# Performance work log

Measured on AMD Instinct MI355X. Metric: run time of the kernel, lower is better.

## Reference

```python
import jax, jax.numpy as jnp
import numpy as np

N, F, V, E = 16384, 39, 100000, 16
H1, H2 = 400, 400
EPS = 1e-5

def setup_inputs() -> dict:
    key = jax.random.key(0)
    ks = jax.random.split(key, 12)
    xi = jax.random.randint(ks[0], (N, F, 1), 0, V)  # indices per field
    xv = jax.random.uniform(ks[1], (N, F), dtype=jnp.float32)
    # stacked per-field embedding tables (each table has V+1 rows)
    emb1 = jax.random.normal(ks[2], (F, V + 1), dtype=jnp.float32)          # 1st-order
    emb2 = jax.random.normal(ks[3], (F, V + 1, E), dtype=jnp.float32)       # 2nd-order
    D = F * E
    W1 = jax.random.normal(ks[4], (D, H1), dtype=jnp.float32) / np.sqrt(D)
    b1 = jnp.zeros((H1,), jnp.float32)
    g1 = jnp.ones((H1,), jnp.float32)
    be1 = jnp.zeros((H1,), jnp.float32)
    W2 = jax.random.normal(ks[5], (H1, H2), dtype=jnp.float32) / np.sqrt(H1)
    b2 = jnp.zeros((H2,), jnp.float32)
    g2 = jnp.ones((H2,), jnp.float32)
    be2 = jnp.zeros((H2,), jnp.float32)
    bias = jax.random.normal(ks[6], (1,), dtype=jnp.float32)
    return dict(xi=xi, xv=xv, emb1=emb1, emb2=emb2, W1=W1, b1=b1, g1=g1, be1=be1,
                W2=W2, b2=b2, g2=g2, be2=be2, bias=bias)

def _batchnorm(x, g, b):
    # BatchNorm1d in training mode: batch mean/var (biased)
    mu = x.mean(0)
    var = x.var(0)
    return g * (x - mu) * jax.lax.rsqrt(var + EPS) + b

def reference(xi, xv, emb1, emb2, W1, b1, g1, be1, W2, b2, g2, be2, bias):
    idx = xi[:, :, 0]                     # (N, F)
    f_ids = jnp.arange(F)[None, :]        # (1, F)
    e1 = emb1[f_ids, idx] * xv            # (N, F): per-field 1st-order term
    e2 = emb2[f_ids, idx] * xv[:, :, None]  # (N, F, E)
    s = e2.sum(axis=1)                    # (N, E) sum of embeddings
    fm2 = 0.5 * (s * s - (e2 * e2).sum(axis=1))  # (N, E) FM 2nd-order
    deep = e2.reshape(e2.shape[0], F * E)
    h = _batchnorm(deep @ W1 + b1, g1, be1)       # dropout = identity (eval)
    h = _batchnorm(h @ W2 + b2, g2, be2)
    return e1.sum(axis=1) + fm2.sum(axis=1) + h.sum(axis=1) + bias[0]
```

## Files before the change

### kernel.cpp

```cpp
#include <hip/hip_runtime.h>
#include <hip/hip_bf16.h>

#define Nn 16384
#define Ff 39
#define Vv 100000
#define Ee 16
#define Dd 624
#define Hh 400
#define EPSf 1e-5f

typedef short short8 __attribute__((ext_vector_type(8)));
typedef float floatx4 __attribute__((ext_vector_type(4)));

__device__ __forceinline__ float bf2f(unsigned short v) {
  union { unsigned int u; float f; } x; x.u = ((unsigned int)v) << 16; return x.f;
}

__global__ __launch_bounds__(256) void embed_kernel(
    const int* __restrict__ xi, const float* __restrict__ xv,
    const float* __restrict__ emb1, const float* __restrict__ emb2,
    const float* __restrict__ bias,
    __hip_bfloat16* __restrict__ deep, float* __restrict__ p) {
  __shared__ int   sidx[4][40];
  __shared__ float sxv[4][40];
  const int w = threadIdx.x >> 6;
  const int lane = threadIdx.x & 63;
  const int n = blockIdx.x * 4 + w;
  if (lane < Ff) {
    sidx[w][lane] = xi[n * Ff + lane];
    sxv[w][lane]  = xv[n * Ff + lane];
  }
  __syncthreads();

  float s_e = 0.f, sq_e = 0.f;
  #pragma unroll
  for (int j = lane; j < Dd; j += 64) {
    const int f = j >> 4;
    const long off = ((long)f * (Vv + 1) + sidx[w][f]) * Ee + (j & 15);
    const float v = emb2[off] * sxv[w][f];
    deep[(long)n * Dd + j] = __float2bfloat16(v);
    s_e += v; sq_e += v * v;
  }
  s_e  += __shfl_xor(s_e, 16);  sq_e += __shfl_xor(sq_e, 16);
  s_e  += __shfl_xor(s_e, 32);  sq_e += __shfl_xor(sq_e, 32);

  float val = (lane < Ee) ? 0.5f * (s_e * s_e - sq_e) : 0.f;
  if (lane < Ff)
    val += emb1[(long)lane * (Vv + 1) + sidx[w][lane]] * sxv[w][lane];
  #pragma unroll
  for (int d = 1; d < 64; d <<= 1) val += __shfl_xor(val, d);
  if (lane == 0) p[n] = val + bias[0];
}

__global__ __launch_bounds__(256) void gemm_bf16(
    const __hip_bfloat16* __restrict__ A, const __hip_bfloat16* __restrict__ Wt,
    const float* __restrict__ bias, __hip_bfloat16* __restrict__ C,
    float* __restrict__ s, float* __restrict__ ss, int K) {
  __shared__ uint4 As4[128 * 5];
  __shared__ uint4 Bs4[80 * 5];
  const int tid = threadIdx.x;
  const int n0 = blockIdx.x * 80;
  const int m0 = blockIdx.y * 128;
  const int w = tid >> 6, lane = tid & 63;
  const int lm = lane & 15, qd = lane >> 4;

  floatx4 acc[2][5];
  #pragma unroll
  for (int i = 0; i < 2; ++i)
    #pragma unroll
    for (int j = 0; j < 5; ++j)
      acc[i][j] = (floatx4){0.f, 0.f, 0.f, 0.f};

  const short* As_s = (const short*)As4;
  const short* Bs_s = (const short*)Bs4;
  const int nk = (K + 31) >> 5;

  for (int ks = 0; ks < nk; ++ks) {
    const int k0 = ks << 5;
    #pragma unroll
    for (int cc = 0; cc < 2; ++cc) {
      const int c = tid + cc * 256;
      const int m = c >> 2, kc = c & 3;
      const int k = k0 + kc * 8;
      uint4 v = make_uint4(0, 0, 0, 0);
      if (k < K) v = *(const uint4*)&A[(size_t)(m0 + m) * K + k];
      As4[m * 5 + kc] = v;
    }
    for (int c = tid; c < 320; c += 256) {
      const int n = c >> 2, kc = c & 3;
      const int k = k0 + kc * 8;
      uint4 v = make_uint4(0, 0, 0, 0);
      if (k < K) v = *(const uint4*)&Wt[(size_t)(n0 + n) * K + k];
      Bs4[n * 5 + kc] = v;
    }
    __syncthreads();
    const short8 a0 = *(const short8*)&As_s[(w * 32 + 0  + lm) * 40 + qd * 8];
    const short8 a1 = *(const short8*)&As_s[(w * 32 + 16 + lm) * 40 + qd * 8];
    #pragma unroll
    for (int nt = 0; nt < 5; ++nt) {
      const short8 b = *(const short8*)&Bs_s[(nt * 16 + lm) * 40 + qd * 8];
      acc[0][nt] = __builtin_amdgcn_mfma_f32_16x16x32_bf16(a0, b, acc[0][nt], 0, 0, 0);
      acc[1][nt] = __builtin_amdgcn_mfma_f32_16x16x32_bf16(a1, b, acc[1][nt], 0, 0, 0);
    }
    __syncthreads();
  }

  const int rb = m0 + w * 32 + qd * 4;
  #pragma unroll
  for (int nt = 0; nt < 5; ++nt) {
    const int col = n0 + nt * 16 + lm;
    const float bc = bias[col];
    float cs = 0.f, cq = 0.f;
    #pragma unroll
    for (int mt = 0; mt < 2; ++mt) {
      #pragma unroll
      for (int r = 0; r < 4; ++r) {
        const float v = acc[mt][nt][r] + bc;
        const __hip_bfloat16 hv = __float2bfloat16(v);
        C[(size_t)(rb + mt * 16 + r) * Hh + col] = hv;
        const float vf = __bfloat162float(hv);
        cs += vf; cq += vf * vf;
      }
    }
    cs += __shfl_xor(cs, 16); cq += __shfl_xor(cq, 16);
    cs += __shfl_xor(cs, 32); cq += __shfl_xor(cq, 32);
    if (lane < 16) { atomicAdd(&s[col], cs); atomicAdd(&ss[col], cq); }
  }
}

__global__ __launch_bounds__(256) void conv1_kernel(
    const float* __restrict__ W1, __hip_bfloat16* __restrict__ W1t) {
  const int n = blockIdx.x, t = threadIdx.x;
  for (int k = t; k < Dd; k += 256)
    W1t[(size_t)n * Dd + k] = __float2bfloat16(W1[(size_t)k * Hh + n]);
}

__global__ void a1c1_kernel(
    const float* __restrict__ s1, const float* __restrict__ ss1,
    const float* __restrict__ g1, const float* __restrict__ be1,
    float* __restrict__ a1, float* __restrict__ c1) {
  const int t = threadIdx.x;
  if (t < Hh) {
    const float mu = s1[t] * (1.f / Nn);
    const float var = ss1[t] * (1.f / Nn) - mu * mu;
    const float a = g1[t] * rsqrtf(var + EPSf);
    a1[t] = a;
    c1[t] = be1[t] - a * mu;
  }
}

__global__ __launch_bounds__(256) void prep2_kernel(
    const float* __restrict__ W2, const float* __restrict__ a1, const float* __restrict__ c1,
    const float* __restrict__ b2, __hip_bfloat16* __restrict__ W2t, float* __restrict__ b2p) {
  __shared__ float red[256];
  const int n = blockIdx.x, t = threadIdx.x;
  float acc = 0.f;
  for (int k = t; k < Hh; k += 256) {
    const float wv = W2[(size_t)k * Hh + n];
    W2t[(size_t)n * Hh + k] = __float2bfloat16(a1[k] * wv);
    acc += c1[k] * wv;
  }
  red[t] = acc; __syncthreads();
  for (int d = 128; d > 0; d >>= 1) { if (t < d) red[t] += red[t + d]; __syncthreads(); }
  if (t == 0) b2p[n] = b2[n] + red[0];
}

__global__ __launch_bounds__(512) void alpha_kernel(
    const float* __restrict__ s2, const float* __restrict__ ss2,
    const float* __restrict__ g2, const float* __restrict__ be2,
    float* __restrict__ alpha, float* __restrict__ c2) {
  __shared__ float red[512];
  const int t = threadIdx.x;
  float part = 0.f;
  if (t < Hh) {
    const float mu = s2[t] * (1.f / Nn);
    const float var = ss2[t] * (1.f / Nn) - mu * mu;
    const float al = g2[t] * rsqrtf(var + EPSf);
    alpha[t] = al;
    part = be2[t] - al * mu;
  }
  red[t] = part;
  __syncthreads();
  for (int d = 256; d > 0; d >>= 1) { if (t < d) red[t] += red[t + d]; __syncthreads(); }
  if (t == 0) c2[0] = red[0];
}

__global__ __launch_bounds__(256) void final_kernel(
    const __hip_bfloat16* __restrict__ x2, const float* __restrict__ alpha,
    const float* __restrict__ p, const float* __restrict__ c2,
    float* __restrict__ out) {
  const int w = threadIdx.x >> 6, lane = threadIdx.x & 63;
  const int n = blockIdx.x * 4 + w;
  const unsigned short* row = (const unsigned short*)(x2 + (size_t)n * Hh);
  float acc = 0.f;
  for (int h0 = lane * 4; h0 < Hh; h0 += 256) {
    const ushort4 u = *(const ushort4*)&row[h0];
    const float4 al = *(const float4*)&alpha[h0];
    acc += bf2f(u.x) * al.x + bf2f(u.y) * al.y + bf2f(u.z) * al.z + bf2f(u.w) * al.w;
  }
  #pragma unroll
  for (int d = 1; d < 64; d <<= 1) acc += __shfl_xor(acc, d);
  if (lane == 0) out[n] = p[n] + acc + c2[0];
}

extern "C" void kernel_launch(void* const* d_in, const int* in_sizes, int n_in,
                              void* d_out, int out_size, void* d_ws, size_t ws_size,
                              hipStream_t stream) {
  const int*   xi   = (const int*)d_in[0];
  const float* xv   = (const float*)d_in[1];
  const float* emb1 = (const float*)d_in[2];
  const float* emb2 = (const float*)d_in[3];
  const float* W1   = (const float*)d_in[4];
  const float* b1   = (const float*)d_in[5];
  const float* g1   = (const float*)d_in[6];
  const float* be1  = (const float*)d_in[7];
  const float* W2   = (const float*)d_in[8];
  const float* b2   = (const float*)d_in[9];
  const float* g2   = (const float*)d_in[10];
  const float* be2  = (const float*)d_in[11];
  const float* bias = (const float*)d_in[12];
  float* out = (float*)d_out;

  char* ws = (char*)d_ws;
  __hip_bfloat16* deep = (__hip_bfloat16*)ws;                  ws += (size_t)Nn * Dd * 2;
  __hip_bfloat16* x1b  = (__hip_bfloat16*)ws;                  ws += (size_t)Nn * Hh * 2;
  __hip_bfloat16* x2b  = (__hip_bfloat16*)ws;                  ws += (size_t)Nn * Hh * 2;
  __hip_bfloat16* W1t  = (__hip_bfloat16*)ws;                  ws += (size_t)Hh * Dd * 2;
  __hip_bfloat16* W2t  = (__hip_bfloat16*)ws;                  ws += (size_t)Hh * Hh * 2;
  float* p    = (float*)ws;  ws += (size_t)Nn * 4;
  float* s1   = (float*)ws;  ws += Hh * 4;
  float* ss1  = (float*)ws;  ws += Hh * 4;
  float* s2   = (float*)ws;  ws += Hh * 4;
  float* ss2  = (float*)ws;  ws += Hh * 4;
  float* a1   = (float*)ws;  ws += Hh * 4;
  float* c1   = (float*)ws;  ws += Hh * 4;
  float* alpha= (float*)ws;  ws += Hh * 4;
  float* b2p  = (float*)ws;  ws += Hh * 4;
  float* c2   = (float*)ws;  ws += 16;

  hipMemsetAsync(s1, 0, 4 * Hh * sizeof(float), stream);

  embed_kernel<<<Nn / 4, 256, 0, stream>>>(xi, xv, emb1, emb2, bias, deep, p);
  conv1_kernel<<<Hh, 256, 0, stream>>>(W1, W1t);

  gemm_bf16<<<dim3(5, Nn / 128), 256, 0, stream>>>(deep, W1t, b1, x1b, s1, ss1, Dd);
  a1c1_kernel<<<1, 512, 0, stream>>>(s1, ss1, g1, be1, a1, c1);
  prep2_kernel<<<Hh, 256, 0, stream>>>(W2, a1, c1, b2, W2t, b2p);

  gemm_bf16<<<dim3(5, Nn / 128), 256, 0, stream>>>(x1b, W2t, b2p, x2b, s2, ss2, Hh);
  alpha_kernel<<<1, 512, 0, stream>>>(s2, ss2, g2, be2, alpha, c2);

  final_kernel<<<Nn / 4, 256, 0, stream>>>(x2b, alpha, p, c2, out);
}
```

Baseline: 440.3 us.

## Fuse small prep kernels into neighbors and double GEMM K-tile to 64

Folds the W1 transpose and the stats zeroing into extra blocks of the embedding kernel, and drops the memset. The BN1 scale/shift computation moves into prep2 and the BN2 alpha/c2 computation into the final kernel, which removes several tiny launches and their serialization gaps. The GEMM now stages a K-step of 64 with padded LDS rows, halving barrier count per tile. In exchange, every final-kernel block recomputes the alpha reduction redundantly. For K=400 the last 64-wide step is partly zero-padded.

Result: no change. 432.5 us (-1.8%).

```diff
diff --git a/kernel.cpp b/kernel.cpp
--- a/kernel.cpp
+++ b/kernel.cpp
@@ -19,13 +19,25 @@
 __global__ __launch_bounds__(256) void embed_kernel(
     const int* __restrict__ xi, const float* __restrict__ xv,
     const float* __restrict__ emb1, const float* __restrict__ emb2,
-    const float* __restrict__ bias,
-    __hip_bfloat16* __restrict__ deep, float* __restrict__ p) {
+    const float* __restrict__ bias, const float* __restrict__ W1,
+    __hip_bfloat16* __restrict__ deep, float* __restrict__ p,
+    __hip_bfloat16* __restrict__ W1t, float* __restrict__ stats) {
+  const int b = blockIdx.x;
+  if (b >= 4096) {
+    if (b == 4496) {
+      for (int i = threadIdx.x; i < 1600; i += 256) stats[i] = 0.f;
+    } else {
+      const int n = b - 4096;
+      for (int k = threadIdx.x; k < Dd; k += 256)
+        W1t[(size_t)n * Dd + k] = __float2bfloat16(W1[(size_t)k * Hh + n]);
+    }
+    return;
+  }
   __shared__ int   sidx[4][40];
   __shared__ float sxv[4][40];
   const int w = threadIdx.x >> 6;
   const int lane = threadIdx.x & 63;
-  const int n = blockIdx.x * 4 + w;
+  const int n = b * 4 + w;
   if (lane < Ff) {
     sidx[w][lane] = xi[n * Ff + lane];
     sxv[w][lane]  = xv[n * Ff + lane];
@@ -56,8 +68,8 @@
     const __hip_bfloat16* __restrict__ A, const __hip_bfloat16* __restrict__ Wt,
     const float* __restrict__ bias, __hip_bfloat16* __restrict__ C,
     float* __restrict__ s, float* __restrict__ ss, int K) {
-  __shared__ uint4 As4[128 * 5];
-  __shared__ uint4 Bs4[80 * 5];
+  __shared__ uint4 As4[128 * 9];
+  __shared__ uint4 Bs4[80 * 9];
   const int tid = threadIdx.x;
   const int n0 = blockIdx.x * 80;
   const int m0 = blockIdx.y * 128;
@@ -73,34 +85,38 @@
 
   const short* As_s = (const short*)As4;
   const short* Bs_s = (const short*)Bs4;
-  const int nk = (K + 31) >> 5;
+  const int nk = (K + 63) >> 6;
 
   for (int ks = 0; ks < nk; ++ks) {
-    const int k0 = ks << 5;
-    #pragma unroll
-    for (int cc = 0; cc < 2; ++cc) {
+    const int k0 = ks << 6;
+    #pragma unroll
+    for (int cc = 0; cc < 4; ++cc) {
       const int c = tid + cc * 256;
-      const int m = c >> 2, kc = c & 3;
+      const int m = c >> 3, kc = c & 7;
       const int k = k0 + kc * 8;
       uint4 v = make_uint4(0, 0, 0, 0);
       if (k < K) v = *(const uint4*)&A[(size_t)(m0 + m) * K + k];
-      As4[m * 5 + kc] = v;
-    }
-    for (int c = tid; c < 320; c += 256) {
-      const int n = c >> 2, kc = c & 3;
+      As4[m * 9 + kc] = v;
+    }
+    for (int c = tid; c < 640; c += 256) {
+      const int n = c >> 3, kc = c & 7;
       const int k = k0 + kc * 8;
       uint4 v = make_uint4(0, 0, 0, 0);
       if (k < K) v = *(const uint4*)&Wt[(size_t)(n0 + n) * K + k];
-      Bs4[n * 5 + kc] = v;
+      Bs4[n * 9 + kc] = v;
     }
     __syncthreads();
-    const short8 a0 = *(const short8*)&As_s[(w * 32 + 0  + lm) * 40 + qd * 8];
-    const short8 a1 = *(const short8*)&As_s[(w * 32 + 16 + lm) * 40 + qd * 8];
-    #pragma unroll
-    for (int nt = 0; nt < 5; ++nt) {
-      const short8 b = *(const short8*)&Bs_s[(nt * 16 + lm) * 40 + qd * 8];
-      acc[0][nt] = __builtin_amdgcn_mfma_f32_16x16x32_bf16(a0, b, acc[0][nt], 0, 0, 0);
-      acc[1][nt] = __builtin_amdgcn_mfma_f32_16x16x32_bf16(a1, b, acc[1][nt], 0, 0, 0);
+    #pragma unroll
+    for (int h = 0; h < 2; ++h) {
+      const int ko = h * 32 + qd * 8;
+      const short8 a0 = *(const short8*)&As_s[(w * 32 + 0  + lm) * 72 + ko];
+      const short8 a1 = *(const short8*)&As_s[(w * 32 + 16 + lm) * 72 + ko];
+      #pragma unroll
+      for (int nt = 0; nt < 5; ++nt) {
+        const short8 b = *(const short8*)&Bs_s[(nt * 16 + lm) * 72 + ko];
+        acc[0][nt] = __builtin_amdgcn_mfma_f32_16x16x32_bf16(a0, b, acc[0][nt], 0, 0, 0);
+        acc[1][nt] = __builtin_amdgcn_mfma_f32_16x16x32_bf16(a1, b, acc[1][nt], 0, 0, 0);
+      }
     }
     __syncthreads();
   }
@@ -128,79 +144,66 @@
   }
 }
 
-__global__ __launch_bounds__(256) void conv1_kernel(
-    const float* __restrict__ W1, __hip_bfloat16* __restrict__ W1t) {
-  const int n = blockIdx.x, t = threadIdx.x;
-  for (int k = t; k < Dd; k += 256)
-    W1t[(size_t)n * Dd + k] = __float2bfloat16(W1[(size_t)k * Hh + n]);
-}
-
-__global__ void a1c1_kernel(
+__global__ __launch_bounds__(256) void prep2_kernel(
+    const float* __restrict__ W2,
     const float* __restrict__ s1, const float* __restrict__ ss1,
     const float* __restrict__ g1, const float* __restrict__ be1,
-    float* __restrict__ a1, float* __restrict__ c1) {
-  const int t = threadIdx.x;
-  if (t < Hh) {
-    const float mu = s1[t] * (1.f / Nn);
-    const float var = ss1[t] * (1.f / Nn) - mu * mu;
-    const float a = g1[t] * rsqrtf(var + EPSf);
-    a1[t] = a;
-    c1[t] = be1[t] - a * mu;
-  }
-}
-
-__global__ __launch_bounds__(256) void prep2_kernel(
-    const float* __restrict__ W2, const float* __restrict__ a1, const float* __restrict__ c1,
     const float* __restrict__ b2, __hip_bfloat16* __restrict__ W2t, float* __restrict__ b2p) {
+  __shared__ float sa1[Hh], sc1[Hh];
   __shared__ float red[256];
   const int n = blockIdx.x, t = threadIdx.x;
+  for (int k = t; k < Hh; k += 256) {
+    const float mu = s1[k] * (1.f / Nn);
+    const float var = ss1[k] * (1.f / Nn) - mu * mu;
+    const float a = g1[k] * rsqrtf(var + EPSf);
+    sa1[k] = a;
+    sc1[k] = be1[k] - a * mu;
+  }
+  __syncthreads();
   float acc = 0.f;
   for (int k = t; k < Hh; k += 256) {
     const float wv = W2[(size_t)k * Hh + n];
-    W2t[(size_t)n * Hh + k] = __float2bfloat16(a1[k] * wv);
-    acc += c1[k] * wv;
+    W2t[(size_t)n * Hh + k] = __float2bfloat16(sa1[k] * wv);
+    acc += sc1[k] * wv;
   }
   red[t] = acc; __syncthreads();
   for (int d = 128; d > 0; d >>= 1) { if (t < d) red[t] += red[t + d]; __syncthreads(); }
   if (t == 0) b2p[n] = b2[n] + red[0];
 }
 
-__global__ __launch_bounds__(512) void alpha_kernel(
+__global__ __launch_bounds__(256) void final_kernel(
+    const __hip_bfloat16* __restrict__ x2,
     const float* __restrict__ s2, const float* __restrict__ ss2,
     const float* __restrict__ g2, const float* __restrict__ be2,
-    float* __restrict__ alpha, float* __restrict__ c2) {
-  __shared__ float red[512];
+    const float* __restrict__ p, float* __restrict__ out) {
+  __shared__ float sal[Hh];
+  __shared__ float red[256];
   const int t = threadIdx.x;
   float part = 0.f;
-  if (t < Hh) {
-    const float mu = s2[t] * (1.f / Nn);
-    const float var = ss2[t] * (1.f / Nn) - mu * mu;
-    const float al = g2[t] * rsqrtf(var + EPSf);
-    alpha[t] = al;
-    part = be2[t] - al * mu;
-  }
-  red[t] = part;
+  for (int h = t; h < Hh; h += 256) {
+    const float mu = s2[h] * (1.f / Nn);
+    const float var = ss2[h] * (1.f / Nn) - mu * mu;
+    const float al = g2[h] * rsqrtf(var + EPSf);
+    sal[h] = al;
+    part += be2[h] - al * mu;
+  }
+  red[t] = part; __syncthreads();
+  for (int d = 128; d > 0; d >>= 1) { if (t < d) red[t] += red[t + d]; __syncthreads(); }
   __syncthreads();
-  for (int d = 256; d > 0; d >>= 1) { if (t < d) red[t] += red[t + d]; __syncthreads(); }
-  if (t == 0) c2[0] = red[0];
-}
-
-__global__ __launch_bounds__(256) void final_kernel(
-    const __hip_bfloat16* __restrict__ x2, const float* __restrict__ alpha,
-    const float* __restrict__ p, const float* __restrict__ c2,
-    float* __restrict__ out) {
-  const int w = threadIdx.x >> 6, lane = threadIdx.x & 63;
+  const float c2 = red[0];
+
+  const int w = t >> 6, lane = t & 63;
   const int n = blockIdx.x * 4 + w;
   const unsigned short* row = (const unsigned short*)(x2 + (size_t)n * Hh);
   float acc = 0.f;
   for (int h0 = lane * 4; h0 < Hh; h0 += 256) {
     const ushort4 u = *(const ushort4*)&row[h0];
-    const float4 al = *(const float4*)&alpha[h0];
-    acc += bf2f(u.x) * al.x + bf2f(u.y) * al.y + bf2f(u.z) * al.z + bf2f(u.w) * al.w;
+    acc += bf2f(u.x) * sal[h0] + bf2f(u.y) * sal[h0 + 1]
+         + bf2f(u.z) * sal[h0 + 2] + bf2f(u.w) * sal[h0 + 3];
   }
   #pragma unroll
   for (int d = 1; d < 64; d <<= 1) acc += __shfl_xor(acc, d);
-  if (lane == 0) out[n] = p[n] + acc + c2[0];
+  if (lane == 0) out[n] = p[n] + acc + c2;
 }
 
 extern "C" void kernel_launch(void* const* d_in, const int* in_sizes, int n_in,
@@ -222,33 +225,21 @@
   float* out = (float*)d_out;
 
   char* ws = (char*)d_ws;
-  __hip_bfloat16* deep = (__hip_bfloat16*)ws;                  ws += (size_t)Nn * Dd * 2;
-  __hip_bfloat16* x1b  = (__hip_bfloat16*)ws;                  ws += (size_t)Nn * Hh * 2;
-  __hip_bfloat16* x2b  = (__hip_bfloat16*)ws;                  ws += (size_t)Nn * Hh * 2;
-  __hip_bfloat16* W1t  = (__hip_bfloat16*)ws;                  ws += (size_t)Hh * Dd * 2;
-  __hip_bfloat16* W2t  = (__hip_bfloat16*)ws;                  ws += (size_t)Hh * Hh * 2;
+  __hip_bfloat16* deep = (__hip_bfloat16*)ws;  ws += (size_t)Nn * Dd * 2;
+  __hip_bfloat16* x1b  = (__hip_bfloat16*)ws;  ws += (size_t)Nn * Hh * 2;
+  __hip_bfloat16* x2b  = (__hip_bfloat16*)ws;  ws += (size_t)Nn * Hh * 2;
+  __hip_bfloat16* W1t  = (__hip_bfloat16*)ws;  ws += (size_t)Hh * Dd * 2;
+  __hip_bfloat16* W2t  = (__hip_bfloat16*)ws;  ws += (size_t)Hh * Hh * 2;
   float* p    = (float*)ws;  ws += (size_t)Nn * 4;
   float* s1   = (float*)ws;  ws += Hh * 4;
   float* ss1  = (float*)ws;  ws += Hh * 4;
   float* s2   = (float*)ws;  ws += Hh * 4;
   float* ss2  = (float*)ws;  ws += Hh * 4;
-  float* a1   = (float*)ws;  ws += Hh * 4;
-  float* c1   = (float*)ws;  ws += Hh * 4;
-  float* alpha= (float*)ws;  ws += Hh * 4;
   float* b2p  = (float*)ws;  ws += Hh * 4;
-  float* c2   = (float*)ws;  ws += 16;
-
-  hipMemsetAsync(s1, 0, 4 * Hh * sizeof(float), stream);
-
-  embed_kernel<<<Nn / 4, 256, 0, stream>>>(xi, xv, emb1, emb2, bias, deep, p);
-  conv1_kernel<<<Hh, 256, 0, stream>>>(W1, W1t);
-
+
+  embed_kernel<<<4497, 256, 0, stream>>>(xi, xv, emb1, emb2, bias, W1, deep, p, W1t, s1);
   gemm_bf16<<<dim3(5, Nn / 128), 256, 0, stream>>>(deep, W1t, b1, x1b, s1, ss1, Dd);
-  a1c1_kernel<<<1, 512, 0, stream>>>(s1, ss1, g1, be1, a1, c1);
-  prep2_kernel<<<Hh, 256, 0, stream>>>(W2, a1, c1, b2, W2t, b2p);
-
+  prep2_kernel<<<Hh, 256, 0, stream>>>(W2, s1, ss1, g1, be1, b2, W2t, b2p);
   gemm_bf16<<<dim3(5, Nn / 128), 256, 0, stream>>>(x1b, W2t, b2p, x2b, s2, ss2, Hh);
-  alpha_kernel<<<1, 512, 0, stream>>>(s2, ss2, g2, be2, alpha, c2);
-
-  final_kernel<<<Nn / 4, 256, 0, stream>>>(x2b, alpha, p, c2, out);
-}
+  final_kernel<<<Nn / 4, 256, 0, stream>>>(x2b, s2, ss2, g2, be2, p, out);
+}
```
